# Optimization experiments

Measured on AMD Instinct MI355X. Metric: run time of the kernel, lower is better.

Reference implementation:

```python
import jax, jax.numpy as jnp
import numpy as np

DIM = 1024
HEADS = 16
EPS = 1e-5  # torch nn.LayerNorm default
SCALE = (DIM / HEADS) ** -0.5


def _layernorm(x, w, b):
    mu = jnp.mean(x, axis=-1, keepdims=True)
    var = jnp.mean((x - mu) ** 2, axis=-1, keepdims=True)
    return (x - mu) * jax.lax.rsqrt(var + EPS) * w + b


def setup_inputs() -> dict:
    key = jax.random.key(0)
    ks = jax.random.split(key, 12)
    B, Lq, Lk, C, g = 2, 1024, 2048, DIM, HEADS
    c = C // g
    inp = {
        "q": jax.random.normal(ks[0], (B, Lq, C), jnp.float32),
        "k": jax.random.normal(ks[1], (B, Lk, C), jnp.float32),
        "v": jax.random.normal(ks[2], (B, Lk, C), jnp.float32),
        "qpos": jax.random.normal(ks[3], (B, Lq, g, c), jnp.float32),
        "kpos": jax.random.normal(ks[4], (B, Lk, g, c), jnp.float32),
        "mask": jax.random.randint(ks[5], (B, 1, 1, Lk), 0, 2, jnp.int32),
        # LayerNorm params
        "ln_q_w": jnp.ones((C,), jnp.float32),
        "ln_q_b": jnp.zeros((C,), jnp.float32),
        "ln_k_w": jnp.ones((C,), jnp.float32),
        "ln_k_b": jnp.zeros((C,), jnp.float32),
        "ln_v_w": jnp.ones((C,), jnp.float32),
        "ln_v_b": jnp.zeros((C,), jnp.float32),
        # Linear weights, torch layout [out, in]; qkv_bias=False
        "w_q": jax.random.normal(ks[6], (C, C), jnp.float32) * 0.02,
        "w_k": jax.random.normal(ks[7], (C, C), jnp.float32) * 0.02,
        "w_v": jax.random.normal(ks[8], (C, C), jnp.float32) * 0.02,
        "w_proj": jax.random.normal(ks[9], (C, C), jnp.float32) * 0.02,
        "b_proj": jnp.zeros((C,), jnp.float32),
    }
    return inp


def reference(q, k, v, qpos, kpos, mask,
              ln_q_w, ln_q_b, ln_k_w, ln_k_b, ln_v_w, ln_v_b,
              w_q, w_k, w_v, w_proj, b_proj):
    B, Lq, C = q.shape
    g = HEADS
    c = C // g
    Lk = k.shape[1]

    # apply_pos: pos is [B, N, g, c]; add per-head then flatten back
    q = (q.reshape(B, Lq, g, c) + qpos).reshape(B, Lq, C)
    k = (k.reshape(B, Lk, g, c) + kpos).reshape(B, Lk, C)

    qn = _layernorm(q, ln_q_w, ln_q_b)
    kn = _layernorm(k, ln_k_w, ln_k_b)
    vn = _layernorm(v, ln_v_w, ln_v_b)

    # torch Linear: x @ W.T
    q4 = jnp.einsum('bnc,dc->bnd', qn, w_q).reshape(B, Lq, g, c)
    k4 = jnp.einsum('bnc,dc->bnd', kn, w_k).reshape(B, Lk, g, c)
    v4 = jnp.einsum('bnc,dc->bnd', vn, w_v).reshape(B, Lk, g, c)

    # scores: [B, q, g, k] (note head dim is axis 2, matching original einsum)
    attn = jnp.einsum('bqgc,bkgc->bqgk', q4, k4) * SCALE
    m = mask.astype(bool)  # [B,1,1,Lk] broadcasts over q and g
    attn = jnp.where(m, -jnp.inf, attn)
    p = jax.nn.softmax(attn, axis=-1)
    p = jnp.where(m, 0.0, p)

    out = jnp.einsum('bqgk,bkgc->bqgc', p, v4).reshape(B, Lq, C)
    out = jnp.einsum('bnc,dc->bnd', out, w_proj) + b_proj
    return out
```

## Files before the change

### kernel.cpp

```cpp
#include <hip/hip_runtime.h>
#include <stdint.h>
#include <stddef.h>

typedef __bf16 bf16;
typedef bf16 bf16x2 __attribute__((ext_vector_type(2)));
typedef bf16 bf16x4 __attribute__((ext_vector_type(4)));
typedef bf16 bf16x8 __attribute__((ext_vector_type(8)));
typedef float f32x4 __attribute__((ext_vector_type(4)));
typedef float f32x16 __attribute__((ext_vector_type(16)));

#define MFMA16(a, b, c) __builtin_amdgcn_mfma_f32_16x16x32_bf16((a), (b), (c), 0, 0, 0)
#define MFMA32(a, b, c) __builtin_amdgcn_mfma_f32_32x32x16_bf16((a), (b), (c), 0, 0, 0)

#define GLD_LDS16(g, l)                                          \
    __builtin_amdgcn_global_load_lds(                            \
        (const __attribute__((address_space(1))) void*)(g),      \
        (__attribute__((address_space(3))) void*)(l), 16, 0, 0)

__global__ __launch_bounds__(256) void cast_all(const float* __restrict__ wq,
                                                const float* __restrict__ wk,
                                                const float* __restrict__ wv,
                                                const float* __restrict__ wp,
                                                bf16* __restrict__ out) {
    int i = (blockIdx.x * 256 + threadIdx.x) * 4;
    const float* src;
    int j = i;
    if (i < (1 << 20)) { src = wq; }
    else if (i < (2 << 20)) { src = wk; j = i - (1 << 20); }
    else if (i < (3 << 20)) { src = wv; j = i - (2 << 20); }
    else { src = wp; j = i - (3 << 20); }
    float4 v = *(const float4*)(src + j);
    bf16x4 o;
    o[0] = (bf16)v.x; o[1] = (bf16)v.y; o[2] = (bf16)v.z; o[3] = (bf16)v.w;
    *(bf16x4*)(out + i) = o;
}

__global__ __launch_bounds__(256) void posln_all(const float* __restrict__ q,
                                                 const float* __restrict__ k,
                                                 const float* __restrict__ v,
                                                 const float* __restrict__ qpos,
                                                 const float* __restrict__ kpos,
                                                 const float* __restrict__ lnqw,
                                                 const float* __restrict__ lnqb,
                                                 const float* __restrict__ lnkw,
                                                 const float* __restrict__ lnkb,
                                                 const float* __restrict__ lnvw,
                                                 const float* __restrict__ lnvb,
                                                 bf16* __restrict__ out) {
    int row = blockIdx.x;
    int t = threadIdx.x;
    const float *x, *pos, *w, *bb;
    int r = row;
    if (row < 2048)      { x = q; pos = qpos; w = lnqw; bb = lnqb; }
    else if (row < 6144) { r = row - 2048; x = k; pos = kpos; w = lnkw; bb = lnkb; }
    else                 { r = row - 6144; x = v; pos = nullptr; w = lnvw; bb = lnvb; }

    float4 vv = ((const float4*)(x + (size_t)r * 1024))[t];
    if (pos != nullptr) {
        float4 p = ((const float4*)(pos + (size_t)r * 1024))[t];
        vv.x += p.x; vv.y += p.y; vv.z += p.z; vv.w += p.w;
    }
    float s1 = vv.x + vv.y + vv.z + vv.w;
    float s2 = vv.x * vv.x + vv.y * vv.y + vv.z * vv.z + vv.w * vv.w;
#pragma unroll
    for (int off = 1; off < 64; off <<= 1) {
        s1 += __shfl_xor(s1, off);
        s2 += __shfl_xor(s2, off);
    }
    __shared__ float red[8];
    int wave = t >> 6;
    if ((t & 63) == 0) { red[wave * 2] = s1; red[wave * 2 + 1] = s2; }
    __syncthreads();
    s1 = red[0] + red[2] + red[4] + red[6];
    s2 = red[1] + red[3] + red[5] + red[7];
    float mu = s1 * (1.0f / 1024.0f);
    float var = s2 * (1.0f / 1024.0f) - mu * mu;
    float rstd = rsqrtf(var + 1e-5f);
    float4 wv4 = ((const float4*)w)[t];
    float4 bv4 = ((const float4*)bb)[t];
    bf16x4 o;
    o[0] = (bf16)((vv.x - mu) * rstd * wv4.x + bv4.x);
    o[1] = (bf16)((vv.y - mu) * rstd * wv4.y + bv4.y);
    o[2] = (bf16)((vv.z - mu) * rstd * wv4.z + bv4.z);
    o[3] = (bf16)((vv.w - mu) * rstd * wv4.w + bv4.w);
    *(bf16x4*)(out + (size_t)row * 1024 + t * 4) = o;
}

template <int BM, typename OutT, bool HasBias, bool VOUT>
__global__ __launch_bounds__(256) void gemm_bt(const bf16* __restrict__ A,
                                               const bf16* __restrict__ w0,
                                               const bf16* __restrict__ w1,
                                               const bf16* __restrict__ w2,
                                               int rowsW0, int rowsW01,
                                               const float* __restrict__ bias,
                                               OutT* __restrict__ out,
                                               bf16* __restrict__ vt) {
    constexpr int MF = 4;
    constexpr int NF = (BM == 128) ? 4 : 2;
    constexpr int WCSPAN = (BM == 128) ? 64 : 32;
    __shared__ bf16 As[BM * 32];
    __shared__ bf16 Bs[128 * 32];
    int bxr = blockIdx.x;
    int bx = (bxr & 7) * (gridDim.x >> 3) + (bxr >> 3);
    int tileN = bx & 7;
    int tileM = bx >> 3;
    int t = threadIdx.x;
    int wave = t >> 6, lane = t & 63;
    int lr = lane & 15, lg = lane >> 4;
    int wr = (BM == 128) ? (wave >> 1) : 0;
    int wc = (BM == 128) ? (wave & 1) : wave;
    int rowBase = tileM * BM;
    const bf16* W = (rowBase < rowsW0) ? w0 : ((rowBase < rowsW01) ? w1 : w2);
    const bf16* Ab = A + (size_t)rowBase * 1024;
    const bf16* Wb = W + (size_t)(tileN * 128) * 1024;

    int o16b0 = wave * 128 + lane;
    int o16b1 = o16b0 + 64;

    const f32x4 zero4 = {0.f, 0.f, 0.f, 0.f};
    f32x4 acc[MF][NF];
#pragma unroll
    for (int i = 0; i < MF; ++i)
#pragma unroll
        for (int j = 0; j < NF; ++j) acc[i][j] = zero4;

    for (int k0 = 0; k0 < 1024; k0 += 32) {
        if constexpr (BM == 128) {
            GLD_LDS16(Ab + (size_t)(o16b0 >> 2) * 1024 + k0 + (o16b0 & 3) * 8,
                      (char*)As + o16b0 * 16);
            GLD_LDS16(Ab + (size_t)(o16b1 >> 2) * 1024 + k0 + (o16b1 & 3) * 8,
                      (char*)As + o16b1 * 16);
        } else {
            GLD_LDS16(Ab + (size_t)(t >> 2) * 1024 + k0 + (t & 3) * 8,
                      (char*)As + t * 16);
        }
        GLD_LDS16(Wb + (size_t)(o16b0 >> 2) * 1024 + k0 + (o16b0 & 3) * 8,
                  (char*)Bs + o16b0 * 16);
        GLD_LDS16(Wb + (size_t)(o16b1 >> 2) * 1024 + k0 + (o16b1 & 3) * 8,
                  (char*)Bs + o16b1 * 16);
        __syncthreads();
        bf16x8 af[MF], bfr[NF];
#pragma unroll
        for (int mf = 0; mf < MF; ++mf)
            af[mf] = *(const bf16x8*)((const char*)As +
                                      (wr * 64 + mf * 16 + lr) * 64 + lg * 16);
#pragma unroll
        for (int nf = 0; nf < NF; ++nf)
            bfr[nf] = *(const bf16x8*)((const char*)Bs +
                                       (wc * WCSPAN + nf * 16 + lr) * 64 + lg * 16);
#pragma unroll
        for (int mf = 0; mf < MF; ++mf)
#pragma unroll
            for (int nf = 0; nf < NF; ++nf)
                acc[mf][nf] = MFMA16(af[mf], bfr[nf], acc[mf][nf]);
        __syncthreads();
    }
    bool isV = VOUT && (rowBase >= 6144);
    if (!isV) {
#pragma unroll
        for (int nf = 0; nf < NF; ++nf) {
            int ncol = tileN * 128 + wc * WCSPAN + nf * 16 + lr;
            float bv = HasBias ? bias[ncol] : 0.0f;
#pragma unroll
            for (int mf = 0; mf < MF; ++mf) {
                int mrow = rowBase + wr * 64 + mf * 16 + lg * 4;
#pragma unroll
                for (int r = 0; r < 4; ++r) {
                    float val = acc[mf][nf][r] + bv;
                    out[(size_t)(mrow + r) * 1024 + ncol] = (OutT)val;
                }
            }
        }
    } else {
        int b2 = (rowBase - 6144) >> 11;
        int kb = rowBase - 6144 - (b2 << 11);
#pragma unroll
        for (int nf = 0; nf < NF; ++nf) {
            int ncol = tileN * 128 + wc * WCSPAN + nf * 16 + lr;
            int h2 = ncol >> 6, d2 = ncol & 63;
            bf16* vrow = vt + ((size_t)((b2 * 16 + h2) * 64 + d2)) * 2048;
#pragma unroll
            for (int mf = 0; mf < MF; ++mf) {
                int kk = kb + wr * 64 + mf * 16 + lg * 4;
                bf16x4 pv;
#pragma unroll
                for (int r = 0; r < 4; ++r) pv[r] = (bf16)acc[mf][nf][r];
                *(bf16x4*)(vrow + kk) = pv;
            }
        }
    }
}

__global__ __launch_bounds__(256, 3) void attn_kernel(const bf16* __restrict__ qkv4,
                                                      const bf16* __restrict__ vt,
                                                      const int* __restrict__ mask,
                                                      bf16* __restrict__ opart,
                                                      float* __restrict__ ml) {
    __shared__ float bias_s[512];
    __shared__ bf16 Ks[2][64 * 64];
    __shared__ bf16 Vs[2][64 * 64];
    int bx = blockIdx.x;
    bx = (bx & 7) * 128 + (bx >> 3);
    int split = bx & 3, qt = (bx >> 2) & 7, h = (bx >> 5) & 15, b = bx >> 9;
    int t = threadIdx.x;
    int wave = t >> 6, lane = t & 63, lq = lane & 31, hi = lane >> 5;
    int lq7 = lq & 7;

    const float SHIFT = 30.0f;
    const int* mrow = mask + b * 2048 + split * 512;
    for (int i = t; i < 512; i += 256) bias_s[i] = mrow[i] ? -1e30f : -SHIFT;

    int qbase = qt * 128 + wave * 32;
    const bf16* qptr = qkv4 + ((size_t)(b * 1024 + qbase + lq)) * 1024 + h * 64 + hi * 8;
    bf16x8 qf[4];
#pragma unroll
    for (int s = 0; s < 4; ++s) qf[s] = *(const bf16x8*)(qptr + s * 16);

    const bf16* kpanel = qkv4 + (size_t)(2048 + b * 2048 + split * 512) * 1024 + h * 64;
    const bf16* vpanel = vt + ((size_t)((b * 16 + h) * 64)) * 2048 + split * 512;

    int r0 = t >> 3, c0 = (t & 7) ^ (r0 & 7);
    int r1 = r0 + 32, c1 = (t & 7) ^ (r1 & 7);

#define STAGE(bufi, lkn)                                                      \
    {                                                                         \
        GLD_LDS16(kpanel + (size_t)((lkn) + r0) * 1024 + c0 * 8,              \
                  (char*)Ks[bufi] + t * 16);                                  \
        GLD_LDS16(kpanel + (size_t)((lkn) + r1) * 1024 + c1 * 8,              \
                  (char*)Ks[bufi] + (t + 256) * 16);                          \
        GLD_LDS16(vpanel + (size_t)r0 * 2048 + (lkn) + c0 * 8,                \
                  (char*)Vs[bufi] + t * 16);                                  \
        GLD_LDS16(vpanel + (size_t)r1 * 2048 + (lkn) + c1 * 8,                \
                  (char*)Vs[bufi] + (t + 256) * 16);                          \
    }

    f32x16 accO0 = {}, accO1 = {};
    float l_run = 0.0f;
    const float C_QK = 0.18033688011112042f;

#define PROCESS(bufi, s2, kloc)                                               \
    {                                                                         \
        const char* kb_ = (const char*)Ks[bufi] + ((s2) * 32 + lq) * 128;     \
        bf16x8 kf0 = *(const bf16x8*)(kb_ + (((hi + 0) ^ lq7) << 4));         \
        bf16x8 kf1 = *(const bf16x8*)(kb_ + (((hi + 2) ^ lq7) << 4));         \
        bf16x8 kf2 = *(const bf16x8*)(kb_ + (((hi + 4) ^ lq7) << 4));         \
        bf16x8 kf3 = *(const bf16x8*)(kb_ + (((hi + 6) ^ lq7) << 4));         \
        f32x16 S = {};                                                        \
        __builtin_amdgcn_s_setprio(1);                                        \
        S = MFMA32(kf0, qf[0], S);                                            \
        S = MFMA32(kf1, qf[1], S);                                            \
        S = MFMA32(kf2, qf[2], S);                                            \
        S = MFMA32(kf3, qf[3], S);                                            \
        __builtin_amdgcn_s_setprio(0);                                        \
        f32x4 bv0 = *(const f32x4*)&bias_s[(kloc) + 4 * hi];                  \
        f32x4 bv1 = *(const f32x4*)&bias_s[(kloc) + 8 + 4 * hi];              \
        f32x4 bv2 = *(const f32x4*)&bias_s[(kloc) + 16 + 4 * hi];             \
        f32x4 bv3 = *(const f32x4*)&bias_s[(kloc) + 24 + 4 * hi];             \
        float p[16];                                                          \
        _Pragma("unroll")                                                     \
        for (int r = 0; r < 16; ++r) {                                        \
            float bvr = (r < 4 ? bv0[r & 3] : r < 8 ? bv1[r & 3]              \
                         : r < 12 ? bv2[r & 3] : bv3[r & 3]);                 \
            p[r] = __builtin_amdgcn_exp2f(fmaf(S[r], C_QK, bvr));             \
        }                                                                     \
        l_run += ((p[0] + p[1]) + (p[2] + p[3])) + ((p[4] + p[5]) + (p[6] + p[7])) \
               + ((p[8] + p[9]) + (p[10] + p[11])) + ((p[12] + p[13]) + (p[14] + p[15])); \
        union { unsigned u[4]; bf16x8 v; } pf0, pf1;                          \
        _Pragma("unroll")                                                     \
        for (int w = 0; w < 4; ++w) {                                         \
            union { bf16x2 h2; unsigned u; } cv;                              \
            cv.h2[0] = (bf16)p[2 * w]; cv.h2[1] = (bf16)p[2 * w + 1];         \
            pf0.u[w] = cv.u;                                                  \
            cv.h2[0] = (bf16)p[8 + 2 * w]; cv.h2[1] = (bf16)p[9 + 2 * w];     \
            pf1.u[w] = cv.u;                                                  \
        }                                                                     \
        const char* vbA = (const char*)Vs[bufi] + lq * 128 + hi * 8;          \
        const char* vbB = vbA + 32 * 128;                                     \
        bf16x4 va[8];                                                         \
        _Pragma("unroll")                                                     \
        for (int m = 0; m < 4; ++m) {                                         \
            int cofs = ((((s2) * 4 + m) ^ lq7) << 4);                         \
            va[m] = *(const bf16x4*)(vbA + cofs);                             \
            va[4 + m] = *(const bf16x4*)(vbB + cofs);                         \
        }                                                                     \
        bf16x8 va0 = __builtin_shufflevector(va[0], va[1], 0, 1, 2, 3, 4, 5, 6, 7); \
        bf16x8 va1 = __builtin_shufflevector(va[2], va[3], 0, 1, 2, 3, 4, 5, 6, 7); \
        bf16x8 va2 = __builtin_shufflevector(va[4], va[5], 0, 1, 2, 3, 4, 5, 6, 7); \
        bf16x8 va3 = __builtin_shufflevector(va[6], va[7], 0, 1, 2, 3, 4, 5, 6, 7); \
        __builtin_amdgcn_s_setprio(1);                                        \
        accO0 = MFMA32(va0, pf0.v, accO0);                                    \
        accO0 = MFMA32(va1, pf1.v, accO0);                                    \
        accO1 = MFMA32(va2, pf0.v, accO1);                                    \
        accO1 = MFMA32(va3, pf1.v, accO1);                                    \
        __builtin_amdgcn_s_setprio(0);                                        \
    }

    STAGE(0, 0);
    __syncthreads();
    int buf = 0;
    for (int it = 0; it < 8; ++it) {
        __builtin_amdgcn_s_barrier();
        if (it < 7) {
            STAGE(buf ^ 1, (it + 1) * 64);
            asm volatile("s_waitcnt vmcnt(4)" ::: "memory");
        } else {
            asm volatile("s_waitcnt vmcnt(0)" ::: "memory");
        }
        __builtin_amdgcn_s_barrier();
        PROCESS(buf, 0, it * 64);
        PROCESS(buf, 1, it * 64 + 32);
        buf ^= 1;
    }
#undef STAGE
#undef PROCESS

    l_run += __shfl_xor(l_run, 32);

    float linv = (l_run > 0.0f) ? (1.0f / l_run) : 0.0f;
    size_t orow = (size_t)(split * 2048 + b * 1024 + qbase + lq);
    bf16* op = opart + orow * 1024 + h * 64;
#pragma unroll
    for (int m = 0; m < 4; ++m) {
        bf16x4 y0, y1;
#pragma unroll
        for (int r = 0; r < 4; ++r) {
            y0[r] = (bf16)(accO0[4 * m + r] * linv);
            y1[r] = (bf16)(accO1[4 * m + r] * linv);
        }
        *(bf16x4*)(op + 8 * m + 4 * hi) = y0;
        *(bf16x4*)(op + 32 + 8 * m + 4 * hi) = y1;
    }
    if (lane < 32) {
        float2 mlv = {SHIFT, l_run};
        *(float2*)(ml + (orow * 16 + h) * 2) = mlv;
    }
}

__global__ __launch_bounds__(256) void combine_kernel(const bf16* __restrict__ opart,
                                                      const float* __restrict__ ml,
                                                      bf16* __restrict__ out) {
    int row = blockIdx.x;
    int t = threadIdx.x;
    int h = t >> 4;
    float m[4], l[4];
#pragma unroll
    for (int s = 0; s < 4; ++s) {
        const float* p = ml + ((size_t)(s * 2048 + row) * 16 + h) * 2;
        m[s] = p[0]; l[s] = p[1];
    }
    float M = fmaxf(fmaxf(m[0], m[1]), fmaxf(m[2], m[3]));
    float u[4], denom = 0.0f;
#pragma unroll
    for (int s = 0; s < 4; ++s) { u[s] = exp2f(m[s] - M) * l[s]; denom += u[s]; }
    float inv = (denom > 0.0f) ? (1.0f / denom) : 0.0f;
    float acc[4] = {0.f, 0.f, 0.f, 0.f};
#pragma unroll
    for (int s = 0; s < 4; ++s) {
        bf16x4 y = *(const bf16x4*)(opart + (size_t)(s * 2048 + row) * 1024 + t * 4);
#pragma unroll
        for (int c = 0; c < 4; ++c) acc[c] += u[s] * (float)y[c];
    }
    bf16x4 r;
#pragma unroll
    for (int c = 0; c < 4; ++c) r[c] = (bf16)(acc[c] * inv);
    *(bf16x4*)(out + (size_t)row * 1024 + t * 4) = r;
}

extern "C" void kernel_launch(void* const* d_in, const int* in_sizes, int n_in,
                              void* d_out, int out_size, void* d_ws, size_t ws_size,
                              hipStream_t stream) {
    const float* q    = (const float*)d_in[0];
    const float* k    = (const float*)d_in[1];
    const float* v    = (const float*)d_in[2];
    const float* qpos = (const float*)d_in[3];
    const float* kpos = (const float*)d_in[4];
    const int*   mask = (const int*)d_in[5];
    const float* lnqw = (const float*)d_in[6];
    const float* lnqb = (const float*)d_in[7];
    const float* lnkw = (const float*)d_in[8];
    const float* lnkb = (const float*)d_in[9];
    const float* lnvw = (const float*)d_in[10];
    const float* lnvb = (const float*)d_in[11];
    const float* wq   = (const float*)d_in[12];
    const float* wk   = (const float*)d_in[13];
    const float* wv   = (const float*)d_in[14];
    const float* wp   = (const float*)d_in[15];
    const float* bp   = (const float*)d_in[16];
    float* out = (float*)d_out;

    char* ws = (char*)d_ws;
    const size_t MB = 1024 * 1024;
    bf16*  wq_b  = (bf16*)(ws + 0 * MB);
    bf16*  wk_b  = (bf16*)(ws + 2 * MB);
    bf16*  wv_b  = (bf16*)(ws + 4 * MB);
    bf16*  wp_b  = (bf16*)(ws + 6 * MB);
    bf16*  xn    = (bf16*)(ws + 8 * MB);
    bf16*  opart = (bf16*)(ws + 8 * MB);
    float* mlbuf = (float*)(ws + 24 * MB);
    bf16*  qkv4  = (bf16*)(ws + 28 * MB);
    bf16*  vtb   = (bf16*)(ws + 40 * MB);
    bf16*  attn  = (bf16*)(ws + 0 * MB);

    cast_all<<<4096, 256, 0, stream>>>(wq, wk, wv, wp, wq_b);

    posln_all<<<10240, 256, 0, stream>>>(q, k, v, qpos, kpos,
                                         lnqw, lnqb, lnkw, lnkb, lnvw, lnvb, xn);

    gemm_bt<128, bf16, false, true><<<640, 256, 0, stream>>>(
        xn, wq_b, wk_b, wv_b, 2048, 6144, nullptr, qkv4, vtb);

    attn_kernel<<<1024, 256, 0, stream>>>(qkv4, vtb, mask, opart, mlbuf);

    combine_kernel<<<2048, 256, 0, stream>>>(opart, mlbuf, attn);

    gemm_bt<64, float, true, false><<<256, 256, 0, stream>>>(
        attn, wp_b, wp_b, wp_b, 1 << 20, 1 << 20, bp, out, nullptr);
}
```

Baseline: 111.0 us.

## Double-buffer GEMM LDS tiles with async prefetch and MFMA priority

The projection GEMM gets a two-stage LDS ring: the next K-slice is issued via global_load_lds while the current slice is consumed, with explicit vmcnt waits and raw barriers replacing the two __syncthreads per iteration. s_setprio is raised around the MFMA block. The goal is to hide global-load latency behind matrix math. The cost is doubled LDS use, which may reduce occupancy, and the correctness of the hand-written wait counts and barrier ordering must hold.

```diff
diff --git a/kernel.cpp b/kernel.cpp
--- a/kernel.cpp
+++ b/kernel.cpp
@@ -98,8 +98,9 @@
     constexpr int MF = 4;
     constexpr int NF = (BM == 128) ? 4 : 2;
     constexpr int WCSPAN = (BM == 128) ? 64 : 32;
-    __shared__ bf16 As[BM * 32];
-    __shared__ bf16 Bs[128 * 32];
+    constexpr int NLOADS = (BM == 128) ? 4 : 3;
+    __shared__ bf16 As[2][BM * 32];
+    __shared__ bf16 Bs[2][128 * 32];
     int bxr = blockIdx.x;
     int bx = (bxr & 7) * (gridDim.x >> 3) + (bxr >> 3);
     int tileN = bx & 7;
@@ -117,6 +118,23 @@
     int o16b0 = wave * 128 + lane;
     int o16b1 = o16b0 + 64;
 
+#define GSTAGE(bufi, k0n)                                                     \
+    {                                                                         \
+        if constexpr (BM == 128) {                                            \
+            GLD_LDS16(Ab + (size_t)(o16b0 >> 2) * 1024 + (k0n) + (o16b0 & 3) * 8, \
+                      (char*)As[bufi] + o16b0 * 16);                          \
+            GLD_LDS16(Ab + (size_t)(o16b1 >> 2) * 1024 + (k0n) + (o16b1 & 3) * 8, \
+                      (char*)As[bufi] + o16b1 * 16);                          \
+        } else {                                                              \
+            GLD_LDS16(Ab + (size_t)(t >> 2) * 1024 + (k0n) + (t & 3) * 8,     \
+                      (char*)As[bufi] + t * 16);                              \
+        }                                                                     \
+        GLD_LDS16(Wb + (size_t)(o16b0 >> 2) * 1024 + (k0n) + (o16b0 & 3) * 8, \
+                  (char*)Bs[bufi] + o16b0 * 16);                              \
+        GLD_LDS16(Wb + (size_t)(o16b1 >> 2) * 1024 + (k0n) + (o16b1 & 3) * 8, \
+                  (char*)Bs[bufi] + o16b1 * 16);                              \
+    }
+
     const f32x4 zero4 = {0.f, 0.f, 0.f, 0.f};
     f32x4 acc[MF][NF];
 #pragma unroll
@@ -124,37 +142,37 @@
 #pragma unroll
         for (int j = 0; j < NF; ++j) acc[i][j] = zero4;
 
+    GSTAGE(0, 0);
+    __syncthreads();
+    int gbuf = 0;
     for (int k0 = 0; k0 < 1024; k0 += 32) {
-        if constexpr (BM == 128) {
-            GLD_LDS16(Ab + (size_t)(o16b0 >> 2) * 1024 + k0 + (o16b0 & 3) * 8,
-                      (char*)As + o16b0 * 16);
-            GLD_LDS16(Ab + (size_t)(o16b1 >> 2) * 1024 + k0 + (o16b1 & 3) * 8,
-                      (char*)As + o16b1 * 16);
+        __builtin_amdgcn_s_barrier();
+        if (k0 + 32 < 1024) {
+            GSTAGE(gbuf ^ 1, k0 + 32);
+            asm volatile("s_waitcnt vmcnt(%0)" :: "i"(NLOADS) : "memory");
         } else {
-            GLD_LDS16(Ab + (size_t)(t >> 2) * 1024 + k0 + (t & 3) * 8,
-                      (char*)As + t * 16);
+            asm volatile("s_waitcnt vmcnt(0)" ::: "memory");
         }
-        GLD_LDS16(Wb + (size_t)(o16b0 >> 2) * 1024 + k0 + (o16b0 & 3) * 8,
-                  (char*)Bs + o16b0 * 16);
-        GLD_LDS16(Wb + (size_t)(o16b1 >> 2) * 1024 + k0 + (o16b1 & 3) * 8,
-                  (char*)Bs + o16b1 * 16);
-        __syncthreads();
+        __builtin_amdgcn_s_barrier();
         bf16x8 af[MF], bfr[NF];
 #pragma unroll
         for (int mf = 0; mf < MF; ++mf)
-            af[mf] = *(const bf16x8*)((const char*)As +
+            af[mf] = *(const bf16x8*)((const char*)As[gbuf] +
                                       (wr * 64 + mf * 16 + lr) * 64 + lg * 16);
 #pragma unroll
         for (int nf = 0; nf < NF; ++nf)
-            bfr[nf] = *(const bf16x8*)((const char*)Bs +
+            bfr[nf] = *(const bf16x8*)((const char*)Bs[gbuf] +
                                        (wc * WCSPAN + nf * 16 + lr) * 64 + lg * 16);
+        __builtin_amdgcn_s_setprio(1);
 #pragma unroll
         for (int mf = 0; mf < MF; ++mf)
 #pragma unroll
             for (int nf = 0; nf < NF; ++nf)
                 acc[mf][nf] = MFMA16(af[mf], bfr[nf], acc[mf][nf]);
-        __syncthreads();
-    }
+        __builtin_amdgcn_s_setprio(0);
+        gbuf ^= 1;
+    }
+#undef GSTAGE
     bool isV = VOUT && (rowBase >= 6144);
     if (!isV) {
 #pragma unroll
```

Result: no change. 112.9 us (+1.7%).
